# Optimization experiments

Measured on AMD Instinct MI355X. Metric: run time of the kernel, lower is better.

## Reference

```python
import jax, jax.numpy as jnp
import numpy as np

HEAD_SIZE = 64
N_EMBED = 768
B, T = 16, 2048


def setup_inputs() -> dict:
    key = jax.random.key(0)
    ks = jax.random.split(key, 7)
    return {
        "x": jax.random.normal(ks[0], (B, T, N_EMBED), dtype=jnp.float32),
        "v1": jax.random.normal(ks[1], (B, T, HEAD_SIZE), dtype=jnp.float32),
        "Wk": jax.random.normal(ks[2], (N_EMBED, HEAD_SIZE), dtype=jnp.float32) * 0.02,
        "Wq": jax.random.normal(ks[3], (N_EMBED, HEAD_SIZE), dtype=jnp.float32) * 0.02,
        "Wv": jax.random.normal(ks[4], (N_EMBED, HEAD_SIZE), dtype=jnp.float32) * 0.02,
        "Wproj": jax.random.normal(ks[5], (HEAD_SIZE, HEAD_SIZE), dtype=jnp.float32) * 0.02,
        "bproj": jnp.zeros((HEAD_SIZE,), dtype=jnp.float32),
        "lamb": jnp.float32(0.5),
    }


def reference(x, v1, Wk, Wq, Wv, Wproj, bproj, lamb):
    # x: [B, T, C]; single-head causal attention with value-residual mixing.
    k = x @ Wk  # [B, T, H]
    q = x @ Wq
    v = x @ Wv
    v = (1.0 - lamb) * v + lamb * v1  # value-residual mix
    scale = jnp.float32(1.0 / np.sqrt(HEAD_SIZE))
    w = jnp.einsum("bth,bsh->bts", q, k) * scale  # [B, T, T]
    t = x.shape[1]
    causal = jnp.tril(jnp.ones((t, t), dtype=bool))  # [T, T]
    w = jnp.where(causal, w, jnp.float32(-jnp.inf))
    w = jax.nn.softmax(w, axis=-1)
    # dropout is identity in eval mode
    out = jnp.einsum("bts,bsh->bth", w, v)  # [B, T, H]
    return out @ Wproj + bproj, v1
```

## Files before the change

kernel.cpp:

```cpp
#include <hip/hip_runtime.h>
#include <hip/hip_bf16.h>


constexpr int BATCH = 16;
constexpr int TSEQ  = 2048;
constexpr int CEMB  = 768;
constexpr int HS    = 64;
constexpr size_t NTOK    = (size_t)BATCH * TSEQ;
constexpr size_t OUTHALF = NTOK * HS;

typedef __bf16 bf16x4 __attribute__((ext_vector_type(4)));
typedef __bf16 bf16x8 __attribute__((ext_vector_type(8)));
typedef float  f32x4  __attribute__((ext_vector_type(4)));
typedef float  f32x16 __attribute__((ext_vector_type(16)));
typedef int    i32x4  __attribute__((ext_vector_type(4)));

__global__ __launch_bounds__(256) void prep_kernel(
    const float* __restrict__ wk, const float* __restrict__ wq,
    const float* __restrict__ wv, const float* __restrict__ wproj,
    __bf16* __restrict__ wt, __bf16* __restrict__ wpt)
{
    __shared__ __bf16 t[64][66];
    const int bid = blockIdx.x;
    if (bid < 36) {
        const int m = bid / 12, c0 = (bid % 12) * 64;
        const float* src = (m == 0) ? wk : (m == 1) ? wq : wv;
        for (int i = threadIdx.x; i < 4096; i += 256) {
            const int c = i >> 6, h = i & 63;
            t[c][h] = (__bf16)src[(size_t)(c0 + c) * HS + h];
        }
        __syncthreads();
        for (int i = threadIdx.x; i < 4096; i += 256) {
            const int h = i >> 6, c = i & 63;
            wt[(size_t)m * HS * CEMB + (size_t)h * CEMB + c0 + c] = t[c][h];
        }
    } else {
        for (int i = threadIdx.x; i < 4096; i += 256) {
            const int h = i >> 6, hp = i & 63;
            t[h][hp] = (__bf16)wproj[i];
        }
        __syncthreads();
        for (int i = threadIdx.x; i < 4096; i += 256) {
            const int hp = i >> 6, h = i & 63;
            wpt[i] = t[h][hp];
        }
    }
}

__global__ __launch_bounds__(256, 4) void qkv_kernel(
    const float* __restrict__ x,
    const float* __restrict__ v1,
    const __bf16* __restrict__ wt,
    const float* __restrict__ lamb_p,
    __bf16* __restrict__ kk,
    __bf16* __restrict__ qq,
    __bf16* __restrict__ vt,
    float* __restrict__ v1out)
{
    __shared__ __bf16 xl[2][32][88];

    const int wave = threadIdx.x >> 6;
    const int lane = threadIdx.x & 63;
    const int l16  = lane & 15;
    const int quad = lane >> 4;
    const size_t row0 = (size_t)blockIdx.x * 32;

    const int tok_s = threadIdx.x >> 3;
    const int cq    = threadIdx.x & 7;
    const float* xsrc = x + (row0 + tok_s) * CEMB + cq * 8;

    const __bf16* wbase[3];
    #pragma unroll
    for (int m = 0; m < 3; ++m)
        wbase[m] = wt + ((size_t)m * HS + wave * 16 + l16) * CEMB + quad * 8;

    f32x4 acc[3][2];
    #pragma unroll
    for (int m = 0; m < 3; ++m)
        #pragma unroll
        for (int rt = 0; rt < 2; ++rt)
            acc[m][rt] = (f32x4){0.f, 0.f, 0.f, 0.f};

    {
        f32x4 t0 = *(const f32x4*)(xsrc);
        f32x4 t1 = *(const f32x4*)(xsrc + 4);
        bf16x8 v;
        #pragma unroll
        for (int i = 0; i < 4; ++i) { v[i] = (__bf16)t0[i]; v[i + 4] = (__bf16)t1[i]; }
        *(bf16x8*)&xl[0][tok_s][cq * 8] = v;
    }
    bf16x8 wc[3][2];
    #pragma unroll
    for (int m = 0; m < 3; ++m)
        #pragma unroll
        for (int ks = 0; ks < 2; ++ks)
            wc[m][ks] = *(const bf16x8*)(wbase[m] + ks * 32);
    __syncthreads();

    for (int c0 = 0; c0 < CEMB; c0 += 64) {
        const int buf = (c0 >> 6) & 1;
        const bool notlast = (c0 + 64 < CEMB);

        f32x4 nx0, nx1;
        bf16x8 wn[3][2];
        if (notlast) {
            const float* xs = xsrc + c0 + 64;
            nx0 = *(const f32x4*)(xs);
            nx1 = *(const f32x4*)(xs + 4);
            #pragma unroll
            for (int m = 0; m < 3; ++m)
                #pragma unroll
                for (int ks = 0; ks < 2; ++ks)
                    wn[m][ks] = *(const bf16x8*)(wbase[m] + c0 + 64 + ks * 32);
        }

        #pragma unroll
        for (int ks = 0; ks < 2; ++ks) {
            bf16x8 a[2];
            #pragma unroll
            for (int rt = 0; rt < 2; ++rt)
                a[rt] = *(const bf16x8*)&xl[buf][rt * 16 + l16][ks * 32 + quad * 8];
            #pragma unroll
            for (int m = 0; m < 3; ++m)
                #pragma unroll
                for (int rt = 0; rt < 2; ++rt)
                    acc[m][rt] = __builtin_amdgcn_mfma_f32_16x16x32_bf16(
                        a[rt], wc[m][ks], acc[m][rt], 0, 0, 0);
        }

        if (notlast) {
            bf16x8 v;
            #pragma unroll
            for (int i = 0; i < 4; ++i) { v[i] = (__bf16)nx0[i]; v[i + 4] = (__bf16)nx1[i]; }
            *(bf16x8*)&xl[buf ^ 1][tok_s][cq * 8] = v;
            #pragma unroll
            for (int m = 0; m < 3; ++m)
                #pragma unroll
                for (int ks = 0; ks < 2; ++ks)
                    wc[m][ks] = wn[m][ks];
            __syncthreads();
        }
    }

    const float lam = lamb_p[0];
    const int col = wave * 16 + l16;
    const int b  = (int)(row0 >> 11);
    __bf16* vtb = vt + (size_t)b * HS * TSEQ + (size_t)col * TSEQ;
    #pragma unroll
    for (int rt = 0; rt < 2; ++rt) {
        const size_t tok0 = row0 + rt * 16 + quad * 4;
        bf16x4 pk;
        #pragma unroll
        for (int r = 0; r < 4; ++r) {
            const size_t idx = (tok0 + r) * HS + col;
            const float v1v = v1[idx];
            kk[idx] = (__bf16)acc[0][rt][r];
            qq[idx] = (__bf16)acc[1][rt][r];
            pk[r] = (__bf16)((1.0f - lam) * acc[2][rt][r] + lam * v1v);
            if (v1out) v1out[idx] = v1v;
        }
        *(bf16x4*)(vtb + (tok0 & 2047)) = pk;
    }
}

__device__ __forceinline__ int pk2(float lo, float hi) {
    unsigned short a = __builtin_bit_cast(unsigned short, (__bf16)lo);
    unsigned short b = __builtin_bit_cast(unsigned short, (__bf16)hi);
    return (int)((((unsigned)b) << 16) | (unsigned)a);
}
__device__ __forceinline__ bf16x8 make_bfrag(const float* p, int hi) {
    const int a0 = pk2(p[0], p[1]), a1 = pk2(p[2], p[3]);
    const int b0 = pk2(p[4], p[5]), b1 = pk2(p[6], p[7]);
    const int pa0 = __shfl_xor(a0, 32), pa1 = __shfl_xor(a1, 32);
    const int pb0 = __shfl_xor(b0, 32), pb1 = __shfl_xor(b1, 32);
    i32x4 w;
    w[0] = hi ? pb0 : a0;
    w[1] = hi ? pb1 : a1;
    w[2] = hi ? b0  : pa0;
    w[3] = hi ? b1  : pa1;
    return __builtin_bit_cast(bf16x8, w);
}

__global__ __launch_bounds__(256, 2) void attn_kernel(
    const __bf16* __restrict__ q,
    const __bf16* __restrict__ k,
    const __bf16* __restrict__ vt,
    const __bf16* __restrict__ wpt,
    const float* __restrict__ bproj,
    float* __restrict__ y)
{
    __shared__ float olds[4][64][32];
    __shared__ float mred[4][32];
    __shared__ float lred[4][32];

    const int b    = blockIdx.x >> 5;
    const int jp   = blockIdx.x & 31;
    const int wave = threadIdx.x >> 6;
    const int lane = threadIdx.x & 63;
    const int l31  = lane & 31;
    const int hi   = lane >> 5;
    const int hi8  = hi * 8;

    const __bf16* kb = k  + (size_t)b * TSEQ * HS;
    const __bf16* vb = vt + (size_t)b * HS * TSEQ;
    const float sc2 = 0.125f * 1.44269504f;

    bf16x8 wf[4];
    if (wave < 2) {
        const __bf16* wp = wpt + (size_t)(wave * 32 + l31) * HS + hi8;
        #pragma unroll
        for (int c = 0; c < 4; ++c) wf[c] = *(const bf16x8*)(wp + c * 16);
    }

    for (int pass = 0; pass < 2; ++pass) {
        const int j = pass ? (63 - jp) : jp;
        const size_t tok0 = (size_t)b * TSEQ + (size_t)j * 32;

        const __bf16* qp = q + (tok0 + l31) * HS + hi8;
        bf16x8 qf[4];
        #pragma unroll
        for (int c = 0; c < 4; ++c) qf[c] = *(const bf16x8*)(qp + c * 16);

        f32x16 o0, o1;
        #pragma unroll
        for (int r = 0; r < 16; ++r) { o0[r] = 0.f; o1[r] = 0.f; }
        float m_i = -1e30f, l_i = 0.f;

        bf16x8 kf[4], kn[4];
        if (wave <= j) {
            const __bf16* kp = kb + (size_t)(wave * 32 + l31) * HS + hi8;
            #pragma unroll
            for (int c = 0; c < 4; ++c) kf[c] = *(const bf16x8*)(kp + c * 16);
        }

        for (int t = wave; t <= j; t += 4) {
            const int s0 = t * 32;
            bf16x8 vf[4];
            #pragma unroll
            for (int ht = 0; ht < 2; ++ht)
                #pragma unroll
                for (int c2 = 0; c2 < 2; ++c2)
                    vf[ht * 2 + c2] = *(const bf16x8*)(vb
                        + (size_t)(ht * 32 + l31) * TSEQ + s0 + c2 * 16 + hi8);
            if (t + 4 <= j) {
                const __bf16* kp = kb + (size_t)((t + 4) * 32 + l31) * HS + hi8;
                #pragma unroll
                for (int c = 0; c < 4; ++c) kn[c] = *(const bf16x8*)(kp + c * 16);
            }

            f32x16 s;
            #pragma unroll
            for (int r = 0; r < 16; ++r) s[r] = 0.f;
            #pragma unroll
            for (int c = 0; c < 4; ++c)
                s = __builtin_amdgcn_mfma_f32_32x32x16_bf16(kf[c], qf[c], s, 0, 0, 0);

            float p[16];
            if (t == j) {
                #pragma unroll
                for (int r = 0; r < 16; ++r) {
                    const int krow = (r & 3) + 8 * (r >> 2) + 4 * hi;
                    p[r] = (krow <= l31) ? s[r] * sc2 : -1e30f;
                }
            } else {
                #pragma unroll
                for (int r = 0; r < 16; ++r) p[r] = s[r] * sc2;
            }

            float x0 = fmaxf(p[0], p[1]),   x1 = fmaxf(p[2], p[3]);
            float x2 = fmaxf(p[4], p[5]),   x3 = fmaxf(p[6], p[7]);
            float x4 = fmaxf(p[8], p[9]),   x5 = fmaxf(p[10], p[11]);
            float x6 = fmaxf(p[12], p[13]), x7 = fmaxf(p[14], p[15]);
            float mx = fmaxf(fmaxf(fmaxf(x0, x1), fmaxf(x2, x3)),
                             fmaxf(fmaxf(x4, x5), fmaxf(x6, x7)));
            mx = fmaxf(mx, __shfl_xor(mx, 32));

            if (!__all(mx <= m_i + 8.f)) {
                const float mn = fmaxf(m_i, mx);
                const float alpha = exp2f(m_i - mn);
                m_i = mn;
                l_i *= alpha;
                #pragma unroll
                for (int r = 0; r < 16; ++r) { o0[r] *= alpha; o1[r] *= alpha; }
            }

            #pragma unroll
            for (int r = 0; r < 16; ++r) p[r] = exp2f(p[r] - m_i);

            float r0 = (p[0] + p[1]) + (p[2] + p[3]);
            float r1 = (p[4] + p[5]) + (p[6] + p[7]);
            float r2 = (p[8] + p[9]) + (p[10] + p[11]);
            float r3 = (p[12] + p[13]) + (p[14] + p[15]);
            float rs = (r0 + r1) + (r2 + r3);
            rs += __shfl_xor(rs, 32);
            l_i += rs;

            const bf16x8 fb0 = make_bfrag(&p[0], hi);
            const bf16x8 fb1 = make_bfrag(&p[8], hi);

            o0 = __builtin_amdgcn_mfma_f32_32x32x16_bf16(vf[0], fb0, o0, 0, 0, 0);
            o0 = __builtin_amdgcn_mfma_f32_32x32x16_bf16(vf[1], fb1, o0, 0, 0, 0);
            o1 = __builtin_amdgcn_mfma_f32_32x32x16_bf16(vf[2], fb0, o1, 0, 0, 0);
            o1 = __builtin_amdgcn_mfma_f32_32x32x16_bf16(vf[3], fb1, o1, 0, 0, 0);

            if (t + 4 <= j) {
                #pragma unroll
                for (int c = 0; c < 4; ++c) kf[c] = kn[c];
            }
        }

        #pragma unroll
        for (int r = 0; r < 16; ++r) {
            const int row = (r & 3) + 8 * (r >> 2) + 4 * hi;
            olds[wave][row][l31]      = o0[r];
            olds[wave][row + 32][l31] = o1[r];
        }
        if (lane < 32) { mred[wave][lane] = m_i; lred[wave][lane] = l_i; }
        __syncthreads();

        if (wave < 2) {
            float mw[4], lw[4];
            #pragma unroll
            for (int w = 0; w < 4; ++w) { mw[w] = mred[w][l31]; lw[w] = lred[w][l31]; }
            const float mg = fmaxf(fmaxf(mw[0], mw[1]), fmaxf(mw[2], mw[3]));
            float g[4], lg = 0.f;
            #pragma unroll
            for (int w = 0; w < 4; ++w) { g[w] = exp2f(mw[w] - mg); lg += g[w] * lw[w]; }
            const float inv = 1.0f / lg;

            float on[32];
            #pragma unroll
            for (int r = 0; r < 16; ++r) {
                const int row = (r & 3) + 8 * (r >> 2) + 4 * hi;
                float a0 = 0.f, a1 = 0.f;
                #pragma unroll
                for (int w = 0; w < 4; ++w) {
                    a0 += g[w] * olds[w][row][l31];
                    a1 += g[w] * olds[w][row + 32][l31];
                }
                on[r]      = a0 * inv;
                on[r + 16] = a1 * inv;
            }

            f32x16 res;
            #pragma unroll
            for (int r = 0; r < 16; ++r) res[r] = 0.f;
            #pragma unroll
            for (int c = 0; c < 4; ++c) {
                const bf16x8 ob = make_bfrag(&on[c * 8], hi);
                res = __builtin_amdgcn_mfma_f32_32x32x16_bf16(wf[c], ob, res, 0, 0, 0);
            }

            float* yp = y + (tok0 + l31) * HS + wave * 32;
            #pragma unroll
            for (int grp = 0; grp < 4; ++grp) {
                const f32x4 bb = *(const f32x4*)(bproj + wave * 32 + grp * 8 + 4 * hi);
                f32x4 o4;
                #pragma unroll
                for (int rr = 0; rr < 4; ++rr) o4[rr] = res[grp * 4 + rr] + bb[rr];
                *(f32x4*)(yp + grp * 8 + 4 * hi) = o4;
            }
        }
        __syncthreads();
    }
}

__global__ __launch_bounds__(256) void copy_kernel(
    const float* __restrict__ src, float* __restrict__ dst)
{
    const size_t i = ((size_t)blockIdx.x * 256 + threadIdx.x) * 4;
    *(f32x4*)(dst + i) = *(const f32x4*)(src + i);
}

extern "C" void kernel_launch(void* const* d_in, const int* in_sizes, int n_in,
                              void* d_out, int out_size, void* d_ws, size_t ws_size,
                              hipStream_t stream) {
    const float* x     = (const float*)d_in[0];
    const float* v1    = (const float*)d_in[1];
    const float* wk    = (const float*)d_in[2];
    const float* wq    = (const float*)d_in[3];
    const float* wv    = (const float*)d_in[4];
    const float* wproj = (const float*)d_in[5];
    const float* bproj = (const float*)d_in[6];
    const float* lamb  = (const float*)d_in[7];

    float* out = (float*)d_out;

    __bf16* qp  = (__bf16*)d_ws;
    __bf16* wt  = qp + OUTHALF;
    __bf16* wpt = wt + (size_t)3 * HS * CEMB;
    const size_t base_elems = OUTHALF + (size_t)3 * HS * CEMB + (size_t)HS * HS;
    const size_t need_bytes = (base_elems + 2 * OUTHALF) * sizeof(__bf16);

    __bf16* kp;
    __bf16* vtp;
    float*  v1out;
    const bool fused_v1 = (ws_size >= need_bytes);
    if (fused_v1) {
        kp    = wpt + (size_t)HS * HS;
        vtp   = kp + OUTHALF;
        v1out = out + OUTHALF;
    } else {
        kp    = (__bf16*)(out + OUTHALF);
        vtp   = kp + OUTHALF;
        v1out = nullptr;
    }

    prep_kernel<<<dim3(37), dim3(256), 0, stream>>>(wk, wq, wv, wproj, wt, wpt);

    qkv_kernel<<<dim3((int)(NTOK / 32)), dim3(256), 0, stream>>>(
        x, v1, wt, lamb, kp, qp, vtp, v1out);

    attn_kernel<<<dim3(BATCH * 32), dim3(256), 0, stream>>>(
        qp, kp, vtp, wpt, bproj, out);

    if (!fused_v1) {
        copy_kernel<<<dim3((int)(OUTHALF / (256 * 4))), dim3(256), 0, stream>>>(
            v1, out + OUTHALF);
    }
}
```

Before: 241.0 us.

## Double QKV projection row tile to 64 tokens and prefetch x two chunks ahead

The QKV projection kernel now processes 64 tokens per block instead of 32, so each weight fragment loaded from global memory feeds twice as many MFMAs. The K loop is unrolled by two with alternating LDS buffers, and x loads are issued two chunks ahead in registers to hide global latency. This raises register use, so launch bounds drop from 4 to 2 blocks per SM, and the grid shrinks to half as many blocks.

```diff
diff --git a/kernel.cpp b/kernel.cpp
--- a/kernel.cpp
+++ b/kernel.cpp
@@ -47,7 +47,7 @@
     }
 }
 
-__global__ __launch_bounds__(256, 4) void qkv_kernel(
+__global__ __launch_bounds__(256, 2) void qkv_kernel(
     const float* __restrict__ x,
     const float* __restrict__ v1,
     const __bf16* __restrict__ wt,
@@ -57,87 +57,97 @@
     __bf16* __restrict__ vt,
     float* __restrict__ v1out)
 {
-    __shared__ __bf16 xl[2][32][88];
+    __shared__ __bf16 xl[2][64][88];
 
     const int wave = threadIdx.x >> 6;
     const int lane = threadIdx.x & 63;
     const int l16  = lane & 15;
     const int quad = lane >> 4;
-    const size_t row0 = (size_t)blockIdx.x * 32;
-
-    const int tok_s = threadIdx.x >> 3;
-    const int cq    = threadIdx.x & 7;
-    const float* xsrc = x + (row0 + tok_s) * CEMB + cq * 8;
+    const size_t row0 = (size_t)blockIdx.x * 64;
+
+    const int tok_s = threadIdx.x >> 2;
+    const int cq    = threadIdx.x & 3;
+    const float* xsrc = x + (row0 + tok_s) * CEMB + cq * 16;
 
     const __bf16* wbase[3];
     #pragma unroll
     for (int m = 0; m < 3; ++m)
         wbase[m] = wt + ((size_t)m * HS + wave * 16 + l16) * CEMB + quad * 8;
 
-    f32x4 acc[3][2];
+    f32x4 acc[3][4];
     #pragma unroll
     for (int m = 0; m < 3; ++m)
         #pragma unroll
-        for (int rt = 0; rt < 2; ++rt)
+        for (int rt = 0; rt < 4; ++rt)
             acc[m][rt] = (f32x4){0.f, 0.f, 0.f, 0.f};
 
+    auto issueX = [&](int chunk, f32x4& a0, f32x4& a1, f32x4& a2, f32x4& a3) {
+        const float* xs = xsrc + chunk * 64;
+        a0 = *(const f32x4*)(xs);
+        a1 = *(const f32x4*)(xs + 4);
+        a2 = *(const f32x4*)(xs + 8);
+        a3 = *(const f32x4*)(xs + 12);
+    };
+    auto writeX = [&](int buf, const f32x4& a0, const f32x4& a1,
+                      const f32x4& a2, const f32x4& a3) {
+        bf16x8 lo, hi;
+        #pragma unroll
+        for (int i = 0; i < 4; ++i) {
+            lo[i] = (__bf16)a0[i]; lo[i + 4] = (__bf16)a1[i];
+            hi[i] = (__bf16)a2[i]; hi[i + 4] = (__bf16)a3[i];
+        }
+        *(bf16x8*)&xl[buf][tok_s][cq * 16]     = lo;
+        *(bf16x8*)&xl[buf][tok_s][cq * 16 + 8] = hi;
+    };
+    auto loadW = [&](int chunk, bf16x8 (&w)[3][2]) {
+        #pragma unroll
+        for (int m = 0; m < 3; ++m)
+            #pragma unroll
+            for (int ks = 0; ks < 2; ++ks)
+                w[m][ks] = *(const bf16x8*)(wbase[m] + chunk * 64 + ks * 32);
+    };
+    auto compute = [&](int buf, const bf16x8 (&w)[3][2]) {
+        #pragma unroll
+        for (int ks = 0; ks < 2; ++ks) {
+            bf16x8 a[4];
+            #pragma unroll
+            for (int rt = 0; rt < 4; ++rt)
+                a[rt] = *(const bf16x8*)&xl[buf][rt * 16 + l16][ks * 32 + quad * 8];
+            #pragma unroll
+            for (int m = 0; m < 3; ++m)
+                #pragma unroll
+                for (int rt = 0; rt < 4; ++rt)
+                    acc[m][rt] = __builtin_amdgcn_mfma_f32_16x16x32_bf16(
+                        a[rt], w[m][ks], acc[m][rt], 0, 0, 0);
+        }
+    };
+
+    f32x4 xa0, xa1, xa2, xa3, xb0, xb1, xb2, xb3;
     {
-        f32x4 t0 = *(const f32x4*)(xsrc);
-        f32x4 t1 = *(const f32x4*)(xsrc + 4);
-        bf16x8 v;
-        #pragma unroll
-        for (int i = 0; i < 4; ++i) { v[i] = (__bf16)t0[i]; v[i + 4] = (__bf16)t1[i]; }
-        *(bf16x8*)&xl[0][tok_s][cq * 8] = v;
-    }
-    bf16x8 wc[3][2];
+        f32x4 t0, t1, t2, t3;
+        issueX(0, t0, t1, t2, t3);
+        writeX(0, t0, t1, t2, t3);
+    }
+    issueX(1, xa0, xa1, xa2, xa3);
+    issueX(2, xb0, xb1, xb2, xb3);
+    bf16x8 wcur[3][2], wnxt[3][2];
+    loadW(0, wcur);
+    __syncthreads();
+
+    constexpr int NCH = CEMB / 64;
     #pragma unroll
-    for (int m = 0; m < 3; ++m)
-        #pragma unroll
-        for (int ks = 0; ks < 2; ++ks)
-            wc[m][ks] = *(const bf16x8*)(wbase[m] + ks * 32);
-    __syncthreads();
-
-    for (int c0 = 0; c0 < CEMB; c0 += 64) {
-        const int buf = (c0 >> 6) & 1;
-        const bool notlast = (c0 + 64 < CEMB);
-
-        f32x4 nx0, nx1;
-        bf16x8 wn[3][2];
-        if (notlast) {
-            const float* xs = xsrc + c0 + 64;
-            nx0 = *(const f32x4*)(xs);
-            nx1 = *(const f32x4*)(xs + 4);
-            #pragma unroll
-            for (int m = 0; m < 3; ++m)
-                #pragma unroll
-                for (int ks = 0; ks < 2; ++ks)
-                    wn[m][ks] = *(const bf16x8*)(wbase[m] + c0 + 64 + ks * 32);
-        }
-
-        #pragma unroll
-        for (int ks = 0; ks < 2; ++ks) {
-            bf16x8 a[2];
-            #pragma unroll
-            for (int rt = 0; rt < 2; ++rt)
-                a[rt] = *(const bf16x8*)&xl[buf][rt * 16 + l16][ks * 32 + quad * 8];
-            #pragma unroll
-            for (int m = 0; m < 3; ++m)
-                #pragma unroll
-                for (int rt = 0; rt < 2; ++rt)
-                    acc[m][rt] = __builtin_amdgcn_mfma_f32_16x16x32_bf16(
-                        a[rt], wc[m][ks], acc[m][rt], 0, 0, 0);
-        }
-
-        if (notlast) {
-            bf16x8 v;
-            #pragma unroll
-            for (int i = 0; i < 4; ++i) { v[i] = (__bf16)nx0[i]; v[i + 4] = (__bf16)nx1[i]; }
-            *(bf16x8*)&xl[buf ^ 1][tok_s][cq * 8] = v;
-            #pragma unroll
-            for (int m = 0; m < 3; ++m)
-                #pragma unroll
-                for (int ks = 0; ks < 2; ++ks)
-                    wc[m][ks] = wn[m][ks];
+    for (int ci = 0; ci < NCH; ci += 2) {
+        loadW(ci + 1, wnxt);
+        compute(0, wcur);
+        writeX(1, xa0, xa1, xa2, xa3);
+        if (ci + 3 < NCH) issueX(ci + 3, xa0, xa1, xa2, xa3);
+        __syncthreads();
+
+        if (ci + 2 < NCH) loadW(ci + 2, wcur);
+        compute(1, wnxt);
+        if (ci + 2 < NCH) {
+            writeX(0, xb0, xb1, xb2, xb3);
+            if (ci + 4 < NCH) issueX(ci + 4, xb0, xb1, xb2, xb3);
             __syncthreads();
         }
     }
@@ -147,7 +157,7 @@
     const int b  = (int)(row0 >> 11);
     __bf16* vtb = vt + (size_t)b * HS * TSEQ + (size_t)col * TSEQ;
     #pragma unroll
-    for (int rt = 0; rt < 2; ++rt) {
+    for (int rt = 0; rt < 4; ++rt) {
         const size_t tok0 = row0 + rt * 16 + quad * 4;
         bf16x4 pk;
         #pragma unroll
@@ -408,7 +418,7 @@
 
     prep_kernel<<<dim3(37), dim3(256), 0, stream>>>(wk, wq, wv, wproj, wt, wpt);
 
-    qkv_kernel<<<dim3((int)(NTOK / 32)), dim3(256), 0, stream>>>(
+    qkv_kernel<<<dim3((int)(NTOK / 64)), dim3(256), 0, stream>>>(
         x, v1, wt, lamb, kp, qp, vtp, v1out);
 
     attn_kernel<<<dim3(BATCH * 32), dim3(256), 0, stream>>>(
```

Measured after the change: 229.4 us. 1.05x faster.
